# Kernel optimization log

Hardware: AMD Instinct MI355X
Metric: run time of the kernel (lower is better)

## Reference

```python
import jax, jax.numpy as jnp
import numpy as np

NUM_RELATIONS = 4
N_NODES = 20000
N_EDGES = 320000
F_IN = 128
HID = 128
EMB = 128


def _rgcn_conv(x, src, dst, edge_type, edge_weight, W, root, bias):
    """One WeightedRGCNConv layer.
    x: [N, in]; W: [R, in, out]; root: [in, out]; bias: [out].
    Math identical to m = einsum('ei,eio->eo', x[src], W[edge_type]) but computed
    as R grouped matmuls to avoid materializing the [E, in, out] weight copy.
    """
    xj = x[src]  # [E, in] gather
    m = jnp.zeros((xj.shape[0], W.shape[2]), dtype=x.dtype)
    for r in range(W.shape[0]):  # fixed small relation count
        mask = (edge_type == r).astype(x.dtype)[:, None]
        m = m + mask * (xj @ W[r])
    m = m * edge_weight[:, None]
    out = jax.ops.segment_sum(m, dst, num_segments=x.shape[0])  # scatter_add
    return out + x @ root + bias


def setup_inputs() -> dict:
    key = jax.random.key(0)
    ks = jax.random.split(key, 10)
    return {
        "x": jax.random.normal(ks[0], (N_NODES, F_IN), dtype=jnp.float32),
        "edge_index": jax.random.randint(ks[1], (2, N_EDGES), 0, N_NODES, dtype=jnp.int64 if jax.config.jax_enable_x64 else jnp.int32).astype(jnp.int32),
        "edge_type": jax.random.randint(ks[2], (N_EDGES,), 0, NUM_RELATIONS).astype(jnp.int32),
        "edge_weight": jax.random.uniform(ks[3], (N_EDGES,), dtype=jnp.float32),
        "W1": jax.random.normal(ks[4], (NUM_RELATIONS, F_IN, HID), dtype=jnp.float32) * 0.05,
        "root1": jax.random.normal(ks[5], (F_IN, HID), dtype=jnp.float32) * 0.05,
        "b1": jax.random.normal(ks[6], (HID,), dtype=jnp.float32) * 0.05,
        "W2": jax.random.normal(ks[7], (NUM_RELATIONS, HID, EMB), dtype=jnp.float32) * 0.05,
        "root2": jax.random.normal(ks[8], (HID, EMB), dtype=jnp.float32) * 0.05,
        "b2": jax.random.normal(ks[9], (EMB,), dtype=jnp.float32) * 0.05,
    }


def reference(x, edge_index, edge_type, edge_weight, W1, root1, b1, W2, root2, b2):
    src, dst = edge_index[0], edge_index[1]
    # min-max normalize edge weights (as in RGCN.forward)
    ew = (edge_weight - edge_weight.min()) / (edge_weight.max() - edge_weight.min() + 1e-08)
    h = jax.nn.relu(_rgcn_conv(x, src, dst, edge_type, ew, W1, root1, b1))
    h = _rgcn_conv(h, src, dst, edge_type, ew, W2, root2, b2)
    return h
```

## Files before the change

### kernel.cpp

```cpp
#include <hip/hip_runtime.h>

#define NN 20000
#define NE 320000
#define FD 128
#define KTOT 640
#define BM 32

typedef float f32x4 __attribute__((ext_vector_type(4)));
typedef __bf16 bf16x8 __attribute__((ext_vector_type(8)));

__device__ __forceinline__ unsigned f2ord(float f) {
  unsigned u = __float_as_uint(f);
  return (u & 0x80000000u) ? ~u : (u | 0x80000000u);
}
__device__ __forceinline__ float ord2f(unsigned u) {
  return (u & 0x80000000u) ? __uint_as_float(u & 0x7FFFFFFFu) : __uint_as_float(~u);
}
__device__ __forceinline__ unsigned pkbf(float a, float b) {
  union { __bf16 h[2]; unsigned u; } p;
  p.h[0] = (__bf16)a; p.h[1] = (__bf16)b; return p.u;
}

__global__ void prep_kernel(unsigned* mm, int* deg,
                            const float* __restrict__ x, unsigned* __restrict__ xb,
                            const float* __restrict__ W1, const float* __restrict__ r1,
                            const float* __restrict__ W2, const float* __restrict__ r2,
                            __bf16* __restrict__ wt1, __bf16* __restrict__ wt2) {
  int i = blockIdx.x * blockDim.x + threadIdx.x;
  if (i == 0) { mm[0] = 0xFFFFFFFFu; mm[1] = 0u; }
  if (i < NN) deg[i] = 0;
  if (i < 2 * FD * KTOT) {
    int which = i / (FD * KTOT);
    int rem = i % (FD * KTOT);
    int n = rem / KTOT, k = rem % KTOT;
    const float* W = which ? W2 : W1;
    const float* rt = which ? r2 : r1;
    float v = (k < 512) ? W[(size_t)k * FD + n] : rt[(size_t)(k - 512) * FD + n];
    (which ? wt2 : wt1)[rem] = (__bf16)v;
  }
  if (i < NN * FD / 4) {
    float4 v = *(const float4*)(x + (size_t)i * 4);
    uint2 p;
    p.x = pkbf(v.x, v.y);
    p.y = pkbf(v.z, v.w);
    *(uint2*)(xb + (size_t)i * 2) = p;
  }
}

__global__ void histmm_kernel(const int* __restrict__ dst, const float* __restrict__ ew,
                              int* deg, unsigned* mm) {
  __shared__ unsigned smn[256], smx[256];
  unsigned lmn = 0xFFFFFFFFu, lmx = 0u;
  for (int i = blockIdx.x * blockDim.x + threadIdx.x; i < NE; i += gridDim.x * blockDim.x) {
    atomicAdd(&deg[dst[i]], 1);
    unsigned o = f2ord(ew[i]);
    lmn = (o < lmn) ? o : lmn;
    lmx = (o > lmx) ? o : lmx;
  }
  smn[threadIdx.x] = lmn; smx[threadIdx.x] = lmx;
  __syncthreads();
  for (int s = 128; s > 0; s >>= 1) {
    if (threadIdx.x < s) {
      unsigned a = smn[threadIdx.x], b = smn[threadIdx.x + s];
      smn[threadIdx.x] = (b < a) ? b : a;
      unsigned c = smx[threadIdx.x], d = smx[threadIdx.x + s];
      smx[threadIdx.x] = (d > c) ? d : c;
    }
    __syncthreads();
  }
  if (threadIdx.x == 0) { atomicMin(&mm[0], smn[0]); atomicMax(&mm[1], smx[0]); }
}

__global__ void scan_kernel(const int* __restrict__ deg, int* offs, int* cursor) {
  __shared__ int part[1024];
  const int CH = (NN + 1023) / 1024;
  int t = threadIdx.x;
  int b = t * CH;
  int e = (b + CH < NN) ? (b + CH) : NN;
  int s = 0;
  for (int i = b; i < e; ++i) s += deg[i];
  part[t] = s;
  __syncthreads();
  for (int off = 1; off < 1024; off <<= 1) {
    int v = part[t];
    int add = (t >= off) ? part[t - off] : 0;
    __syncthreads();
    part[t] = v + add;
    __syncthreads();
  }
  int excl = (t == 0) ? 0 : part[t - 1];
  for (int i = b; i < e; ++i) { offs[i] = excl; cursor[i] = excl; excl += deg[i]; }
  if (t == 1023) offs[NN] = part[1023];
}

__global__ void fill_kernel(const int* __restrict__ src, const int* __restrict__ dst,
                            const int* __restrict__ et, const float* __restrict__ ew,
                            const unsigned* __restrict__ mm, int* cursor,
                            int2* __restrict__ ed) {
  int e = blockIdx.x * blockDim.x + threadIdx.x;
  if (e >= NE) return;
  float mn = ord2f(mm[0]), mx = ord2f(mm[1]);
  float inv = 1.0f / (mx - mn + 1e-8f);
  int d = dst[e];
  int pos = atomicAdd(&cursor[d], 1);
  ed[pos] = make_int2(src[e] | (et[e] << 28), __float_as_int((ew[e] - mn) * inv));
}

__global__ __launch_bounds__(256) void aggregate_kernel(
    const unsigned* __restrict__ xb,
    const int* __restrict__ offs, const int2* __restrict__ ed,
    unsigned* __restrict__ g) {
  int node = (int)((blockIdx.x * blockDim.x + threadIdx.x) >> 6);
  int lane = threadIdx.x & 63;
  if (node >= NN) return;
  int half = lane >> 5, l = lane & 31;
  int beg = offs[node], end = offs[node + 1];
  f32x4 a0 = {0.f, 0.f, 0.f, 0.f}, a1 = a0, a2 = a0, a3 = a0;

#define GAT(E, U)                                                        \
  do {                                                                   \
    int s_ = (E).x & 0x0FFFFFFF;                                         \
    U = *(const uint2*)(xb + (size_t)s_ * 64 + l * 2);                   \
  } while (0)
#define ACCW(E, U, WV)                                                   \
  do {                                                                   \
    float p0 = __uint_as_float((U).x << 16);                             \
    float p1 = __uint_as_float((U).x & 0xFFFF0000u);                     \
    float p2 = __uint_as_float((U).y << 16);                             \
    float p3 = __uint_as_float((U).y & 0xFFFF0000u);                     \
    unsigned r_ = ((unsigned)(E).x) >> 28;                               \
    float w0 = (r_ == 0) ? (WV) : 0.f, w1 = (r_ == 1) ? (WV) : 0.f;      \
    float w2 = (r_ == 2) ? (WV) : 0.f, w3 = (r_ == 3) ? (WV) : 0.f;      \
    a0[0] += w0 * p0; a0[1] += w0 * p1; a0[2] += w0 * p2; a0[3] += w0 * p3; \
    a1[0] += w1 * p0; a1[1] += w1 * p1; a1[2] += w1 * p2; a1[3] += w1 * p3; \
    a2[0] += w2 * p0; a2[1] += w2 * p1; a2[2] += w2 * p2; a2[3] += w2 * p3; \
    a3[0] += w3 * p0; a3[1] += w3 * p1; a3[2] += w3 * p2; a3[3] += w3 * p3; \
  } while (0)

  int j2 = beg;
  if (j2 + 4 <= end) {
    int2 eA = ed[j2 + half];
    int2 eB = ed[j2 + 2 + half];
    do {
      uint2 uA, uB;
      GAT(eA, uA);
      GAT(eB, uB);
      int2 eA2 = ed[j2 + 4 + half];
      int2 eB2 = ed[j2 + 6 + half];
      ACCW(eA, uA, __int_as_float(eA.y));
      ACCW(eB, uB, __int_as_float(eB.y));
      eA = eA2; eB = eB2;
      j2 += 4;
    } while (j2 + 4 <= end);
  }
  for (; j2 < end; j2 += 2) {
    int je = j2 + half;
    int2 e = ed[(je < end) ? je : (end - 1)];
    float wv = (je < end) ? __int_as_float(e.y) : 0.f;
    uint2 u;
    GAT(e, u);
    ACCW(e, u, wv);
  }
#undef GAT
#undef ACCW

#pragma unroll
  for (int q = 0; q < 4; ++q) {
    a0[q] += __shfl_xor(a0[q], 32, 64);
    a1[q] += __shfl_xor(a1[q], 32, 64);
    a2[q] += __shfl_xor(a2[q], 32, 64);
    a3[q] += __shfl_xor(a3[q], 32, 64);
  }

  unsigned* row = g + (size_t)node * 320;
  f32x4 va = half ? a2 : a0;
  f32x4 vb = half ? a3 : a1;
  int r01 = half * 2;
  uint2 w0 = make_uint2(pkbf(va[0], va[1]), pkbf(va[2], va[3]));
  *(uint2*)(row + r01 * 64 + l * 2) = w0;
  uint2 w1 = make_uint2(pkbf(vb[0], vb[1]), pkbf(vb[2], vb[3]));
  *(uint2*)(row + (r01 + 1) * 64 + l * 2) = w1;
  row[256 + lane] = xb[(size_t)node * 64 + lane];
}

template <int BF16OUT>
__global__ __launch_bounds__(512, 2) void gemm_kernel(
    const unsigned* __restrict__ gA,
    const __bf16* __restrict__ wt, const float* __restrict__ bias,
    float* __restrict__ outf, __bf16* __restrict__ outb) {
  __shared__ unsigned As32[BM * 320];
  int tid = threadIdx.x;
  int wave = tid >> 6, lane = tid & 63;
  int wr = wave >> 2, wc = wave & 3;
  int m0 = blockIdx.x * BM;
  int rl = wr * 16 + (lane & 15);
  int kfe = (lane >> 4) * 8;
  int c0 = wc * 32 + (lane & 15);
  const f32x4 zz = {0.f, 0.f, 0.f, 0.f};

  unsigned rowpack = 0, colpack0 = 0, colpack1 = 0;
  {
    if (tid < 256) {
      int row = tid >> 3;
      int wl = (tid & 7) * 2;
      unsigned val = pkbf((float)row * 0.03125f, (float)row * 0.03125f);
      int sw2 = (row & 7) << 2;
      As32[row * 320 + (wl ^ sw2)] = val;
      As32[row * 320 + ((wl + 1) ^ sw2)] = val;
    }
    __syncthreads();
    const char* Arow = (const char*)As32 + rl * 1280;
    int swb = (rl & 7) << 4;
    bf16x8 pa = *(const bf16x8*)(Arow + ((kfe * 2) ^ swb));
    bf16x8 ones, bp0, bp1;
#pragma unroll
    for (int i = 0; i < 8; ++i) ones[i] = (__bf16)1.0f;
    __bf16 c0v = (__bf16)((float)c0 * 0.0078125f);
    __bf16 c1v = (__bf16)((float)(c0 + 16) * 0.0078125f);
#pragma unroll
    for (int i = 0; i < 8; ++i) { bp0[i] = c0v; bp1[i] = c1v; }
    f32x4 P1 = __builtin_amdgcn_mfma_f32_16x16x32_bf16(pa, ones, zz, 0, 0, 0);
    f32x4 P2a = __builtin_amdgcn_mfma_f32_16x16x32_bf16(ones, bp0, zz, 0, 0, 0);
    f32x4 P2b = __builtin_amdgcn_mfma_f32_16x16x32_bf16(ones, bp1, zz, 0, 0, 0);
#pragma unroll
    for (int j = 0; j < 4; ++j) {
      rowpack |= ((unsigned)(int)(P1[j] + 0.5f)) << (8 * j);
      colpack0 |= ((unsigned)(int)(P2a[j] * 4.0f + 0.5f)) << (8 * j);
      colpack1 |= ((unsigned)(int)(P2b[j] * 4.0f + 0.5f)) << (8 * j);
    }
    __syncthreads();
  }

  {
    int row = tid >> 4;
    int c16 = tid & 15;
    const uint4* srcp = (const uint4*)(gA + (size_t)(m0 + row) * 320);
    unsigned sw2 = (row & 7) << 2;
    unsigned* dstw = As32 + row * 320;
#pragma unroll
    for (int jj = 0; jj < 5; ++jj) {
      int chunk = c16 + 16 * jj;
      uint4 v = srcp[chunk];
      *(uint4*)(dstw + ((chunk * 4) ^ sw2)) = v;
    }
  }
  __syncthreads();

  f32x4 acc0 = zz, acc1 = zz;
  const __bf16* w0p = wt + (size_t)c0 * KTOT + kfe;
  const __bf16* w1p = w0p + 16 * KTOT;
  const char* Arow = (const char*)As32 + rl * 1280;
  int swb = (rl & 7) << 4;
#pragma unroll
  for (int step = 0; step < 20; ++step) {
    int b = (step * 64 + kfe * 2) ^ swb;
    bf16x8 a = *(const bf16x8*)(Arow + b);
    bf16x8 b0 = *(const bf16x8*)(w0p + step * 32);
    bf16x8 b1 = *(const bf16x8*)(w1p + step * 32);
    acc0 = __builtin_amdgcn_mfma_f32_16x16x32_bf16(a, b0, acc0, 0, 0, 0);
    acc1 = __builtin_amdgcn_mfma_f32_16x16x32_bf16(a, b1, acc1, 0, 0, 0);
  }

#pragma unroll
  for (int j = 0; j < 4; ++j) {
    int rloc = (int)((rowpack >> (8 * j)) & 255u);
    size_t m = (size_t)(m0 + rloc);
    {
      int col = (int)((colpack0 >> (8 * j)) & 255u);
      float v = acc0[j] + bias[col];
      if (BF16OUT) outb[m * FD + col] = (__bf16)fmaxf(v, 0.f);
      else outf[m * FD + col] = v;
    }
    {
      int col = (int)((colpack1 >> (8 * j)) & 255u);
      float v = acc1[j] + bias[col];
      if (BF16OUT) outb[m * FD + col] = (__bf16)fmaxf(v, 0.f);
      else outf[m * FD + col] = v;
    }
  }
}

extern "C" void kernel_launch(void* const* d_in, const int* in_sizes, int n_in,
                              void* d_out, int out_size, void* d_ws, size_t ws_size,
                              hipStream_t stream) {
  const float* x  = (const float*)d_in[0];
  const int*   ei = (const int*)d_in[1];
  const int*   et = (const int*)d_in[2];
  const float* ew = (const float*)d_in[3];
  const float* W1 = (const float*)d_in[4];
  const float* r1 = (const float*)d_in[5];
  const float* b1 = (const float*)d_in[6];
  const float* W2 = (const float*)d_in[7];
  const float* r2 = (const float*)d_in[8];
  const float* b2 = (const float*)d_in[9];
  float* out = (float*)d_out;
  const int* src = ei;
  const int* dst = ei + NE;

  char* w = (char*)d_ws;
  size_t o = 0;
  auto take = [&](size_t bytes) -> char* {
    char* p = w + o;
    o += (bytes + 255) & ~(size_t)255;
    return p;
  };
  unsigned* mm  = (unsigned*)take(8);
  int* deg      = (int*)take((size_t)NN * 4);
  int* offs     = (int*)take((size_t)(NN + 1) * 4);
  int* cursor   = (int*)take((size_t)NN * 4);
  int2* ed      = (int2*)take((size_t)(NE + 8) * 8);
  unsigned* xb  = (unsigned*)take((size_t)NN * 64 * 4);
  unsigned* g   = (unsigned*)take((size_t)NN * 320 * 4);
  __bf16* h1    = (__bf16*)take((size_t)NN * FD * 2);
  __bf16* wt1   = (__bf16*)take((size_t)FD * KTOT * 2);
  __bf16* wt2   = (__bf16*)take((size_t)FD * KTOT * 2);
  (void)ws_size; (void)n_in; (void)in_sizes; (void)out_size;

  hipLaunchKernelGGL(prep_kernel, dim3((NN * FD / 4 + 255) / 256), dim3(256), 0, stream,
                     mm, deg, x, xb, W1, r1, W2, r2, wt1, wt2);
  hipLaunchKernelGGL(histmm_kernel, dim3(512), dim3(256), 0, stream, dst, ew, deg, mm);
  hipLaunchKernelGGL(scan_kernel, dim3(1), dim3(1024), 0, stream, deg, offs, cursor);
  hipLaunchKernelGGL(fill_kernel, dim3((NE + 255) / 256), dim3(256), 0, stream,
                     src, dst, et, ew, mm, cursor, ed);
  hipLaunchKernelGGL(aggregate_kernel, dim3(NN / 4), dim3(256), 0, stream, xb, offs, ed, g);
  hipLaunchKernelGGL((gemm_kernel<1>), dim3(NN / BM), dim3(512), 0, stream,
                     g, wt1, b1, (float*)nullptr, h1);
  hipLaunchKernelGGL(aggregate_kernel, dim3(NN / 4), dim3(256), 0, stream,
                     (const unsigned*)h1, offs, ed, g);
  hipLaunchKernelGGL((gemm_kernel<0>), dim3(NN / BM), dim3(512), 0, stream,
                     g, wt2, b2, out, (__bf16*)nullptr);
}
```

Measured before the change: 192.5 us.

## Aggregate each node with a full block of four waves and LDS reduction

The aggregation kernel now assigns one 256-thread block per destination node instead of one wave per node. Each of the four waves strides over the node's edges with four independent gathers in flight, each lane reading one packed bf16 pair per edge. Partial sums are then reduced through shared memory by wave 0. This raises memory-level parallelism for the gathers, at the cost of 20000 blocks, a __syncthreads per node, and three idle waves during the reduction and write. With about 16 edges per node, each wave handles only about four edges.

```diff
diff --git a/kernel.cpp b/kernel.cpp
--- a/kernel.cpp
+++ b/kernel.cpp
@@ -110,77 +110,73 @@
     const unsigned* __restrict__ xb,
     const int* __restrict__ offs, const int2* __restrict__ ed,
     unsigned* __restrict__ g) {
-  int node = (int)((blockIdx.x * blockDim.x + threadIdx.x) >> 6);
-  int lane = threadIdx.x & 63;
-  if (node >= NN) return;
-  int half = lane >> 5, l = lane & 31;
+  __shared__ float2 part[3][4][64];
+  int node = blockIdx.x;
+  int wave = threadIdx.x >> 6, lane = threadIdx.x & 63;
   int beg = offs[node], end = offs[node + 1];
-  f32x4 a0 = {0.f, 0.f, 0.f, 0.f}, a1 = a0, a2 = a0, a3 = a0;
-
-#define GAT(E, U)                                                        \
-  do {                                                                   \
-    int s_ = (E).x & 0x0FFFFFFF;                                         \
-    U = *(const uint2*)(xb + (size_t)s_ * 64 + l * 2);                   \
-  } while (0)
+  float a00 = 0.f, a01 = 0.f, a10 = 0.f, a11 = 0.f;
+  float a20 = 0.f, a21 = 0.f, a30 = 0.f, a31 = 0.f;
+
 #define ACCW(E, U, WV)                                                   \
   do {                                                                   \
-    float p0 = __uint_as_float((U).x << 16);                             \
-    float p1 = __uint_as_float((U).x & 0xFFFF0000u);                     \
-    float p2 = __uint_as_float((U).y << 16);                             \
-    float p3 = __uint_as_float((U).y & 0xFFFF0000u);                     \
-    unsigned r_ = ((unsigned)(E).x) >> 28;                               \
-    float w0 = (r_ == 0) ? (WV) : 0.f, w1 = (r_ == 1) ? (WV) : 0.f;      \
-    float w2 = (r_ == 2) ? (WV) : 0.f, w3 = (r_ == 3) ? (WV) : 0.f;      \
-    a0[0] += w0 * p0; a0[1] += w0 * p1; a0[2] += w0 * p2; a0[3] += w0 * p3; \
-    a1[0] += w1 * p0; a1[1] += w1 * p1; a1[2] += w1 * p2; a1[3] += w1 * p3; \
-    a2[0] += w2 * p0; a2[1] += w2 * p1; a2[2] += w2 * p2; a2[3] += w2 * p3; \
-    a3[0] += w3 * p0; a3[1] += w3 * p1; a3[2] += w3 * p2; a3[3] += w3 * p3; \
+    float zp0_ = __uint_as_float((U) << 16);                             \
+    float zp1_ = __uint_as_float((U) & 0xFFFF0000u);                     \
+    unsigned zr_ = ((unsigned)(E).x) >> 28;                              \
+    float zw0_ = (zr_ == 0) ? (WV) : 0.f;                                \
+    float zw1_ = (zr_ == 1) ? (WV) : 0.f;                                \
+    float zw2_ = (zr_ == 2) ? (WV) : 0.f;                                \
+    float zw3_ = (zr_ == 3) ? (WV) : 0.f;                                \
+    a00 += zw0_ * zp0_; a01 += zw0_ * zp1_;                              \
+    a10 += zw1_ * zp0_; a11 += zw1_ * zp1_;                              \
+    a20 += zw2_ * zp0_; a21 += zw2_ * zp1_;                              \
+    a30 += zw3_ * zp0_; a31 += zw3_ * zp1_;                              \
   } while (0)
 
-  int j2 = beg;
-  if (j2 + 4 <= end) {
-    int2 eA = ed[j2 + half];
-    int2 eB = ed[j2 + 2 + half];
-    do {
-      uint2 uA, uB;
-      GAT(eA, uA);
-      GAT(eB, uB);
-      int2 eA2 = ed[j2 + 4 + half];
-      int2 eB2 = ed[j2 + 6 + half];
-      ACCW(eA, uA, __int_as_float(eA.y));
-      ACCW(eB, uB, __int_as_float(eB.y));
-      eA = eA2; eB = eB2;
-      j2 += 4;
-    } while (j2 + 4 <= end);
-  }
-  for (; j2 < end; j2 += 2) {
-    int je = j2 + half;
-    int2 e = ed[(je < end) ? je : (end - 1)];
-    float wv = (je < end) ? __int_as_float(e.y) : 0.f;
-    uint2 u;
-    GAT(e, u);
-    ACCW(e, u, wv);
-  }
-#undef GAT
+  for (int j = beg + wave; j < end; j += 16) {
+    bool v1 = (j + 4) < end, v2 = (j + 8) < end, v3 = (j + 12) < end;
+    int2 e0 = ed[j];
+    int2 e1 = ed[v1 ? j + 4 : j];
+    int2 e2 = ed[v2 ? j + 8 : j];
+    int2 e3 = ed[v3 ? j + 12 : j];
+    unsigned u0 = xb[(size_t)(e0.x & 0x0FFFFFFF) * 64 + lane];
+    unsigned u1 = xb[(size_t)(e1.x & 0x0FFFFFFF) * 64 + lane];
+    unsigned u2 = xb[(size_t)(e2.x & 0x0FFFFFFF) * 64 + lane];
+    unsigned u3 = xb[(size_t)(e3.x & 0x0FFFFFFF) * 64 + lane];
+    float wgt0 = __int_as_float(e0.y);
+    float wgt1 = v1 ? __int_as_float(e1.y) : 0.f;
+    float wgt2 = v2 ? __int_as_float(e2.y) : 0.f;
+    float wgt3 = v3 ? __int_as_float(e3.y) : 0.f;
+    ACCW(e0, u0, wgt0);
+    ACCW(e1, u1, wgt1);
+    ACCW(e2, u2, wgt2);
+    ACCW(e3, u3, wgt3);
+  }
 #undef ACCW
 
-#pragma unroll
-  for (int q = 0; q < 4; ++q) {
-    a0[q] += __shfl_xor(a0[q], 32, 64);
-    a1[q] += __shfl_xor(a1[q], 32, 64);
-    a2[q] += __shfl_xor(a2[q], 32, 64);
-    a3[q] += __shfl_xor(a3[q], 32, 64);
-  }
-
-  unsigned* row = g + (size_t)node * 320;
-  f32x4 va = half ? a2 : a0;
-  f32x4 vb = half ? a3 : a1;
-  int r01 = half * 2;
-  uint2 w0 = make_uint2(pkbf(va[0], va[1]), pkbf(va[2], va[3]));
-  *(uint2*)(row + r01 * 64 + l * 2) = w0;
-  uint2 w1 = make_uint2(pkbf(vb[0], vb[1]), pkbf(vb[2], vb[3]));
-  *(uint2*)(row + (r01 + 1) * 64 + l * 2) = w1;
-  row[256 + lane] = xb[(size_t)node * 64 + lane];
+  if (wave) {
+    part[wave - 1][0][lane] = make_float2(a00, a01);
+    part[wave - 1][1][lane] = make_float2(a10, a11);
+    part[wave - 1][2][lane] = make_float2(a20, a21);
+    part[wave - 1][3][lane] = make_float2(a30, a31);
+  }
+  __syncthreads();
+  if (wave == 0) {
+#pragma unroll
+    for (int w = 0; w < 3; ++w) {
+      float2 q0 = part[w][0][lane], q1 = part[w][1][lane];
+      float2 q2 = part[w][2][lane], q3 = part[w][3][lane];
+      a00 += q0.x; a01 += q0.y;
+      a10 += q1.x; a11 += q1.y;
+      a20 += q2.x; a21 += q2.y;
+      a30 += q3.x; a31 += q3.y;
+    }
+    unsigned* row = g + (size_t)node * 320;
+    row[0 * 64 + lane] = pkbf(a00, a01);
+    row[1 * 64 + lane] = pkbf(a10, a11);
+    row[2 * 64 + lane] = pkbf(a20, a21);
+    row[3 * 64 + lane] = pkbf(a30, a31);
+    row[256 + lane] = xb[(size_t)node * 64 + lane];
+  }
 }
 
 template <int BF16OUT>
@@ -322,10 +318,10 @@
   hipLaunchKernelGGL(scan_kernel, dim3(1), dim3(1024), 0, stream, deg, offs, cursor);
   hipLaunchKernelGGL(fill_kernel, dim3((NE + 255) / 256), dim3(256), 0, stream,
                      src, dst, et, ew, mm, cursor, ed);
-  hipLaunchKernelGGL(aggregate_kernel, dim3(NN / 4), dim3(256), 0, stream, xb, offs, ed, g);
+  hipLaunchKernelGGL(aggregate_kernel, dim3(NN), dim3(256), 0, stream, xb, offs, ed, g);
   hipLaunchKernelGGL((gemm_kernel<1>), dim3(NN / BM), dim3(512), 0, stream,
                      g, wt1, b1, (float*)nullptr, h1);
-  hipLaunchKernelGGL(aggregate_kernel, dim3(NN / 4), dim3(256), 0, stream,
+  hipLaunchKernelGGL(aggregate_kernel, dim3(NN), dim3(256), 0, stream,
                      (const unsigned*)h1, offs, ed, g);
   hipLaunchKernelGGL((gemm_kernel<0>), dim3(NN / BM), dim3(512), 0, stream,
                      g, wt2, b2, out, (__bf16*)nullptr);
```

New measurement: 203.2 us. +5.6%, slower.
